# Kernel tuning notes

Measured on AMD Instinct MI355X. Metric: run time of the kernel, lower is better.

## Reference

```python
import jax, jax.numpy as jnp
import numpy as np

NUM_GROUPS = 512
GROUP_SIZE = 32
GROUP_RADIUS = 0.2
K_ORIGINAL = 5 * GROUP_SIZE  # ball_query oversampling factor from the source


def setup_inputs() -> dict:
    key = jax.random.key(0)
    k1, k2 = jax.random.split(key)
    B, N, C = 8, 16384, 4
    points = jax.random.normal(k1, (B, N, C), dtype=jnp.float32)
    # valid lengths in [N//2, N) so the lengths-masking path is exercised
    lengths = (N // 2 + jax.random.randint(k2, (B,), 0, N // 2)).astype(jnp.int32)
    return {"points": points, "lengths": lengths}


def _sample_farthest_points(xyz, lengths, K):
    # xyz: (B,N,3) float, lengths: (B,) int -> centers (B,K,3)
    B, N, _ = xyz.shape
    n_idx = jnp.arange(N)

    def per_batch(pts, length):
        valid = n_idx < length

        def step(carry, _):
            mindist, cur = carry
            d = jnp.sum((pts - pts[cur]) ** 2, axis=-1)  # (N,)
            mindist = jnp.where(valid, jnp.minimum(mindist, d), -jnp.inf)
            nxt = jnp.argmax(mindist).astype(jnp.int32)
            return (mindist, nxt), cur

        mindist0 = jnp.where(valid, jnp.inf, -jnp.inf)
        # deterministic start at index 0 (source uses random_start_point=True)
        (_, _), sel = jax.lax.scan(step, (mindist0, jnp.int32(0)), None, length=K)
        return pts[sel]

    return jax.vmap(per_batch)(xyz, lengths)


def _ball_query(centers, xyz, lengths, K, radius):
    # returns first-K (by point index, matching pytorch3d ball_query) indices
    # within radius; -1 padding. centers (B,G,3), xyz (B,N,3) -> idx (B,G,K)
    B, G, _ = centers.shape
    N = xyz.shape[1]
    d2 = jnp.sum((centers[:, :, None, :] - xyz[:, None, :, :]) ** 2, axis=-1)  # (B,G,N)
    valid = (jnp.arange(N) < lengths[:, None])[:, None, :]  # (B,1,N)
    mask = (d2 < radius * radius) & valid
    # score N-n > 0 iff in ball; top_k picks smallest indices first (in order)
    score = jnp.where(mask, N - jnp.arange(N, dtype=jnp.int32), jnp.int32(-1))
    vals, _ = jax.lax.top_k(score, K)
    return jnp.where(vals > 0, N - vals, -1)  # (B,G,K)


def _select_topk_by_energy(points, idx, K_new):
    # points (B,N,C), idx (B,G,K_orig) with -1 invalid -> (B,G,K_new)
    B, G, _ = idx.shape
    N = points.shape[1]
    invalid = idx == -1
    idxc = jnp.maximum(idx, 0)
    energies = jnp.broadcast_to(points[:, None, :, 3], (B, G, N))
    e = jnp.take_along_axis(energies, idxc, axis=2)  # (B,G,K_orig)
    e = jnp.where(invalid, -jnp.inf, e)
    top_e, top_i = jax.lax.top_k(e, K_new)
    topk_idx = jnp.take_along_axis(idx, top_i, axis=2)
    return jnp.where(top_e == -jnp.inf, -1, topk_idx)


def _masked_gather(points, idx):
    # points (B,N,C), idx (B,G,K); -1 -> gathered value 0.0 (pytorch3d semantics)
    B, G, K = idx.shape
    C = points.shape[-1]
    valid = idx >= 0
    flat = jnp.maximum(idx, 0).reshape(B, G * K)
    g = jnp.take_along_axis(points, flat[:, :, None], axis=1).reshape(B, G, K, C)
    return jnp.where(valid[..., None], g, 0.0)


def _forward(points, lengths):
    xyz = points[:, :, :3]
    centers = _sample_farthest_points(xyz, lengths, NUM_GROUPS)  # (B,G,3)
    idx = _ball_query(centers, xyz, lengths, K_ORIGINAL, GROUP_RADIUS)
    idx = _select_topk_by_energy(points, idx, GROUP_SIZE)  # (B,G,K)
    # fill_empty_indices: replace -1 with first index of the group
    first = idx[:, :, :1]
    idx = jnp.where(idx == -1, first, idx)
    groups = _masked_gather(points, idx)  # (B,G,K,C)
    groups = jnp.concatenate(
        [groups[..., :3] - centers[:, :, None, :], groups[..., 3:]], axis=-1
    )
    groups = groups / GROUP_RADIUS
    return groups, centers


def reference(points, lengths):
    return _forward(points, lengths)
```

## Files before the change

### kernel.cpp

```cpp
#include <hip/hip_runtime.h>

constexpr int B_ = 8;
constexpr int N_ = 16384;
constexpr int NG = 512;
constexpr int GS = 32;
constexpr int KORIG = 160;
constexpr int TPB = 1024;
constexpr int PPT = 16;
#define R2 0.04f
#define RADIUS 0.2f

typedef __attribute__((ext_vector_type(2))) float f32x2;
typedef __attribute__((ext_vector_type(4))) float f32x4;

__device__ __forceinline__ unsigned f32_ord(float f) {
  unsigned u = __float_as_uint(f);
  return (u & 0x80000000u) ? ~u : (u | 0x80000000u);
}

__device__ __forceinline__ f32x2 pk_add(f32x2 a, f32x2 b) {
  f32x2 d;
  asm("v_pk_add_f32 %0, %1, %2" : "=v"(d) : "v"(a), "v"(b));
  return d;
}
__device__ __forceinline__ f32x2 pk_mul(f32x2 a, f32x2 b) {
  f32x2 d;
  asm("v_pk_mul_f32 %0, %1, %2" : "=v"(d) : "v"(a), "v"(b));
  return d;
}

template <int CTRL>
__device__ __forceinline__ float dpp_fmax(float v) {
  int o = __builtin_amdgcn_update_dpp(0, __float_as_int(v), CTRL, 0xF, 0xF, true);
  return fmaxf(v, __int_as_float(o));
}
__device__ __forceinline__ float wave_fmax(float v) {
  v = dpp_fmax<0xB1>(v);
  v = dpp_fmax<0x4E>(v);
  v = dpp_fmax<0x141>(v);
  v = dpp_fmax<0x140>(v);
  v = fmaxf(v, __int_as_float(__builtin_amdgcn_ds_swizzle(__float_as_int(v), 0x401F)));
  v = fmaxf(v, __shfl_xor(v, 32, 64));
  return v;
}
__device__ __forceinline__ float group16_fmax(float v) {
  v = dpp_fmax<0xB1>(v);
  v = dpp_fmax<0x4E>(v);
  v = dpp_fmax<0x141>(v);
  v = dpp_fmax<0x140>(v);
  return v;
}

__global__ __launch_bounds__(1024, 4) void fps_kernel(const float4* __restrict__ p4,
                                                      const int* __restrict__ lengths,
                                                      float* __restrict__ centers) {
#pragma clang fp contract(off)
  const int b = blockIdx.x;
  const int t = threadIdx.x;
  const int lane = t & 63;
  const int wid = t >> 6;
  const int len = lengths[b];
  const float4* bp = p4 + (size_t)b * N_;
  const float INF = __builtin_inff();

  __shared__ f32x4 sxy4[16 * 8 * 64];
  __shared__ float pubf[2][16];
  __shared__ int pubi[2][16];

  const int base4 = wid * 512 + lane;

  f32x2 z2[8], m2[8];
#pragma unroll
  for (int p = 0; p < 8; ++p) {
    const int i0 = t * PPT + 2 * p;
    float4 a = bp[i0];
    float4 c = bp[i0 + 1];
    sxy4[base4 + p * 64] = (f32x4){a.x, c.x, a.y, c.y};
    z2[p] = (f32x2){a.z, c.z};
    m2[p].x = (i0 < len) ? INF : -INF;
    m2[p].y = (i0 + 1 < len) ? INF : -INF;
  }
  __syncthreads();

  float4 c0 = bp[0];
  float cx = c0.x, cy = c0.y, cz = c0.z;
  if (t == 0) {
    size_t o = (size_t)b * NG * 3;
    centers[o] = cx; centers[o + 1] = cy; centers[o + 2] = cz;
  }

  for (int k = 0; k < NG - 1; ++k) {
    const f32x2 mcx = {-cx, -cx};
    const f32x2 mcy = {-cy, -cy};
    const f32x2 mcz = {-cz, -cz};
#pragma unroll
    for (int p = 0; p < 8; ++p) {
      f32x4 q = sxy4[base4 + p * 64];
      f32x2 xx = pk_add(q.xy, mcx);
      f32x2 yy = pk_add(q.zw, mcy);
      f32x2 zz = pk_add(z2[p], mcz);
      f32x2 x2 = pk_mul(xx, xx);
      f32x2 y2 = pk_mul(yy, yy);
      f32x2 s1 = pk_add(x2, y2);
      f32x2 zq = pk_mul(zz, zz);
      f32x2 d2 = pk_add(s1, zq);
      m2[p].x = fminf(m2[p].x, d2.x);
      m2[p].y = fminf(m2[p].y, d2.y);
    }
    float p0 = fmaxf(m2[0].x, m2[0].y), p1 = fmaxf(m2[1].x, m2[1].y);
    float p2 = fmaxf(m2[2].x, m2[2].y), p3 = fmaxf(m2[3].x, m2[3].y);
    float p4_ = fmaxf(m2[4].x, m2[4].y), p5 = fmaxf(m2[5].x, m2[5].y);
    float p6 = fmaxf(m2[6].x, m2[6].y), p7 = fmaxf(m2[7].x, m2[7].y);
    float r0 = fmaxf(p0, p1), r1 = fmaxf(p2, p3);
    float r2 = fmaxf(p4_, p5), r3 = fmaxf(p6, p7);
    float s0 = fmaxf(r0, r1), s1 = fmaxf(r2, r3);
    const float sm = fmaxf(s0, s1);

    const bool bA = (s0 != sm);
    const float rA = bA ? r2 : r0;
    const bool bB = (rA != sm);
    const float qA = bA ? (bB ? p6 : p4_) : (bB ? p2 : p0);
    const bool bC = (qA != sm);
    const int jp = ((int)bA << 2) | ((int)bB << 1) | (int)bC;
    const float xlo = bA ? (bB ? (bC ? m2[7].x : m2[6].x) : (bC ? m2[5].x : m2[4].x))
                         : (bB ? (bC ? m2[3].x : m2[2].x) : (bC ? m2[1].x : m2[0].x));
    const bool blo = (xlo != sm);
    const int bj = (jp << 1) | (int)blo;

    const float wmax = wave_fmax(sm);
    const unsigned long long att = __ballot(sm == wmax);
    const int wl = __ffsll(att) - 1;
    if (lane == wl) {
      pubf[k & 1][wid] = wmax;
      pubi[k & 1][wid] = t * PPT + bj;
    }
    __syncthreads();

    const float pw = pubf[k & 1][lane & 15];
    const float kmax = group16_fmax(pw);
    const unsigned long long bal = __ballot(pw == kmax);
    const int grp = lane & 48;
    const int ww = __ffsll((bal >> grp) & 0xFFFFull) - 1;
    const int nxt = pubi[k & 1][ww];
    const int snxt = __builtin_amdgcn_readfirstlane(nxt);
    const float4 c = bp[snxt];
    cx = c.x; cy = c.y; cz = c.z;

    if (t == 0) {
      size_t o = ((size_t)b * NG + (k + 1)) * 3;
      centers[o] = cx; centers[o + 1] = cy; centers[o + 2] = cz;
    }
  }
}

__global__ __launch_bounds__(64) void group_kernel(const float4* __restrict__ p4,
                                                   const int* __restrict__ lengths,
                                                   const float* __restrict__ centers,
                                                   float4* __restrict__ outg) {
#pragma clang fp contract(off)
  const int gid = blockIdx.x;
  const int b = gid >> 9;
  const int lane = threadIdx.x;
  const int len = lengths[b];
  const float4* bp = p4 + (size_t)b * N_;
  const float cx = centers[(size_t)gid * 3 + 0];
  const float cy = centers[(size_t)gid * 3 + 1];
  const float cz = centers[(size_t)gid * 3 + 2];

  __shared__ int cand[KORIG];
  int M = 0;
  for (int cb = 0; cb < N_ && M < KORIG; cb += 256) {
#pragma unroll
    for (int q = 0; q < 4; ++q) {
      const int i = cb + q * 64 + lane;
      float4 p = bp[i];
      float dx = p.x - cx;
      float dy = p.y - cy;
      float dz = p.z - cz;
      float d2 = dx * dx + dy * dy + dz * dz;
      const bool pred = (i < len) && (d2 < R2);
      unsigned long long mb = __ballot(pred);
      if (pred) {
        int pos = M + (int)__popcll(mb & ((1ull << lane) - 1ull));
        if (pos < KORIG) cand[pos] = i;
      }
      M += (int)__popcll(mb);
    }
  }
  if (M > KORIG) M = KORIG;
  __syncthreads();

  const unsigned long long SENT = ~0ull;
  unsigned long long key0 = SENT, key1 = SENT, key2 = SENT;
  {
    int c0 = lane, c1 = lane + 64, c2 = lane + 128;
    if (c0 < M) { int i = cand[c0]; key0 = ((unsigned long long)(~f32_ord(bp[i].w)) << 32) | (unsigned)i; }
    if (c1 < M) { int i = cand[c1]; key1 = ((unsigned long long)(~f32_ord(bp[i].w)) << 32) | (unsigned)i; }
    if (c2 < M) { int i = cand[c2]; key2 = ((unsigned long long)(~f32_ord(bp[i].w)) << 32) | (unsigned)i; }
  }

  int mysel = -1;
  for (int j = 0; j < GS; ++j) {
    unsigned long long kmin = key0 < key1 ? key0 : key1;
    if (key2 < kmin) kmin = key2;
#pragma unroll
    for (int off = 32; off > 0; off >>= 1) {
      unsigned long long o = __shfl_xor(kmin, off, 64);
      if (o < kmin) kmin = o;
    }
    if (kmin == SENT) break;
    if (lane == j) mysel = (int)(unsigned)kmin;
    if (key0 == kmin) key0 = SENT;
    if (key1 == kmin) key1 = SENT;
    if (key2 == kmin) key2 = SENT;
  }

  const int first = __shfl(mysel, 0, 64);
  if (lane < GS) {
    int idx = (mysel < 0) ? first : mysel;
    float4 o;
    if (idx >= 0) {
      float4 p = bp[idx];
      o.x = (p.x - cx) / RADIUS;
      o.y = (p.y - cy) / RADIUS;
      o.z = (p.z - cz) / RADIUS;
      o.w = p.w / RADIUS;
    } else {
      o.x = (0.0f - cx) / RADIUS;
      o.y = (0.0f - cy) / RADIUS;
      o.z = (0.0f - cz) / RADIUS;
      o.w = 0.0f;
    }
    outg[(size_t)gid * GS + lane] = o;
  }
}

extern "C" void kernel_launch(void* const* d_in, const int* in_sizes, int n_in,
                              void* d_out, int out_size, void* d_ws, size_t ws_size,
                              hipStream_t stream) {
  const float4* pts = (const float4*)d_in[0];
  const int* lengths = (const int*)d_in[1];
  float* out = (float*)d_out;
  float* centers = out + (size_t)B_ * NG * GS * 4;
  float4* groups = (float4*)out;

  fps_kernel<<<B_, TPB, 0, stream>>>(pts, lengths, centers);
  group_kernel<<<B_ * NG, 64, 0, stream>>>(pts, lengths, centers, groups);
}
```

Baseline: 933.3 us.

## Publish winner coordinates through LDS instead of reloading the point from global memory

In the FPS loop, each wave's winning lane now writes its point's x, y, z coordinates (taken from registers and LDS) together with the max distance into a float4 in shared memory. The next center is then read with shuffles, so the dependent global load of bp[snxt] on the serial critical path of every iteration is gone. Center outputs are buffered in shared memory and written to global memory once after the loop, rather than by a single thread on every iteration. The cost is some extra per-iteration select logic and one more LDS read to fetch the winning coordinates.

```diff
diff --git a/kernel.cpp b/kernel.cpp
--- a/kernel.cpp
+++ b/kernel.cpp
@@ -64,8 +64,8 @@
   const float INF = __builtin_inff();
 
   __shared__ f32x4 sxy4[16 * 8 * 64];
-  __shared__ float pubf[2][16];
-  __shared__ int pubi[2][16];
+  __shared__ f32x4 pub4[2][16];
+  __shared__ float scen[NG * 3];
 
   const int base4 = wid * 512 + lane;
 
@@ -80,14 +80,13 @@
     m2[p].x = (i0 < len) ? INF : -INF;
     m2[p].y = (i0 + 1 < len) ? INF : -INF;
   }
-  __syncthreads();
 
   float4 c0 = bp[0];
   float cx = c0.x, cy = c0.y, cz = c0.z;
   if (t == 0) {
-    size_t o = (size_t)b * NG * 3;
-    centers[o] = cx; centers[o + 1] = cy; centers[o + 2] = cz;
-  }
+    scen[0] = cx; scen[1] = cy; scen[2] = cz;
+  }
+  __syncthreads();
 
   for (int k = 0; k < NG - 1; ++k) {
     const f32x2 mcx = {-cx, -cx};
@@ -125,32 +124,39 @@
     const float xlo = bA ? (bB ? (bC ? m2[7].x : m2[6].x) : (bC ? m2[5].x : m2[4].x))
                          : (bB ? (bC ? m2[3].x : m2[2].x) : (bC ? m2[1].x : m2[0].x));
     const bool blo = (xlo != sm);
-    const int bj = (jp << 1) | (int)blo;
+
+    f32x4 qq = sxy4[base4 + jp * 64];
+    const float gx = blo ? qq.y : qq.x;
+    const float gy = blo ? qq.w : qq.z;
+    const f32x2 zp = bA ? (bB ? (bC ? z2[7] : z2[6]) : (bC ? z2[5] : z2[4]))
+                        : (bB ? (bC ? z2[3] : z2[2]) : (bC ? z2[1] : z2[0]));
+    const float gz = blo ? zp.y : zp.x;
 
     const float wmax = wave_fmax(sm);
     const unsigned long long att = __ballot(sm == wmax);
     const int wl = __ffsll(att) - 1;
-    if (lane == wl) {
-      pubf[k & 1][wid] = wmax;
-      pubi[k & 1][wid] = t * PPT + bj;
-    }
+    if (lane == wl) pub4[k & 1][wid] = (f32x4){wmax, gx, gy, gz};
     __syncthreads();
 
-    const float pw = pubf[k & 1][lane & 15];
-    const float kmax = group16_fmax(pw);
-    const unsigned long long bal = __ballot(pw == kmax);
+    const f32x4 pv = pub4[k & 1][lane & 15];
+    const float kmax = group16_fmax(pv.x);
+    const unsigned long long bal = __ballot(pv.x == kmax);
     const int grp = lane & 48;
-    const int ww = __ffsll((bal >> grp) & 0xFFFFull) - 1;
-    const int nxt = pubi[k & 1][ww];
-    const int snxt = __builtin_amdgcn_readfirstlane(nxt);
-    const float4 c = bp[snxt];
-    cx = c.x; cy = c.y; cz = c.z;
+    const int src = grp + (__ffsll((bal >> grp) & 0xFFFFull) - 1);
+    cx = __shfl(pv.y, src, 64);
+    cy = __shfl(pv.z, src, 64);
+    cz = __shfl(pv.w, src, 64);
 
     if (t == 0) {
-      size_t o = ((size_t)b * NG + (k + 1)) * 3;
-      centers[o] = cx; centers[o + 1] = cy; centers[o + 2] = cz;
-    }
-  }
+      scen[(k + 1) * 3 + 0] = cx;
+      scen[(k + 1) * 3 + 1] = cy;
+      scen[(k + 1) * 3 + 2] = cz;
+    }
+  }
+  __syncthreads();
+
+  float* cb = centers + (size_t)b * NG * 3;
+  for (int i = t; i < NG * 3; i += TPB) cb[i] = scen[i];
 }
 
 __global__ __launch_bounds__(64) void group_kernel(const float4* __restrict__ p4,
```

Result: slower. 971.3 us (+4.1%).

## Shrink FPS block to four waves and replace barrier with tagged atomic publish

Applied to the files above, without the earlier changes.

The farthest-point-sampling kernel now runs 256 threads, each holding 64 points in registers instead of 16, which widens the per-thread reduction tree to 32 pairs. The per-iteration __syncthreads and 16-wave second-stage reduction are replaced by each wave atomically publishing a packed (ordered max, iteration tag, index) word. Waves spin until all four slots carry the current iteration tag. This aims to cut barrier and cross-wave reduction latency in the serial 511-step loop. In exchange there is less latency hiding per SIMD, much higher register pressure, and reliance on spin-wait memory ordering.

```diff
diff --git a/kernel.cpp b/kernel.cpp
--- a/kernel.cpp
+++ b/kernel.cpp
@@ -5,8 +5,8 @@
 constexpr int NG = 512;
 constexpr int GS = 32;
 constexpr int KORIG = 160;
-constexpr int TPB = 1024;
-constexpr int PPT = 16;
+constexpr int TPB = 256;
+constexpr int PPT = 64;
 #define R2 0.04f
 #define RADIUS 0.2f
 
@@ -33,6 +33,11 @@
 __device__ __forceinline__ float dpp_fmax(float v) {
   int o = __builtin_amdgcn_update_dpp(0, __float_as_int(v), CTRL, 0xF, 0xF, true);
   return fmaxf(v, __int_as_float(o));
+}
+template <int CTRL>
+__device__ __forceinline__ unsigned dpp_umax(unsigned v) {
+  int o = __builtin_amdgcn_update_dpp(0, (int)v, CTRL, 0xF, 0xF, true);
+  return v > (unsigned)o ? v : (unsigned)o;
 }
 __device__ __forceinline__ float wave_fmax(float v) {
   v = dpp_fmax<0xB1>(v);
@@ -43,17 +48,12 @@
   v = fmaxf(v, __shfl_xor(v, 32, 64));
   return v;
 }
-__device__ __forceinline__ float group16_fmax(float v) {
-  v = dpp_fmax<0xB1>(v);
-  v = dpp_fmax<0x4E>(v);
-  v = dpp_fmax<0x141>(v);
-  v = dpp_fmax<0x140>(v);
-  return v;
-}
-
-__global__ __launch_bounds__(1024, 4) void fps_kernel(const float4* __restrict__ p4,
-                                                      const int* __restrict__ lengths,
-                                                      float* __restrict__ centers) {
+
+__global__ __attribute__((amdgpu_flat_work_group_size(256, 256),
+                          amdgpu_waves_per_eu(1, 1)))
+void fps_kernel(const float4* __restrict__ p4,
+                const int* __restrict__ lengths,
+                float* __restrict__ centers) {
 #pragma clang fp contract(off)
   const int b = blockIdx.x;
   const int t = threadIdx.x;
@@ -63,15 +63,14 @@
   const float4* bp = p4 + (size_t)b * N_;
   const float INF = __builtin_inff();
 
-  __shared__ f32x4 sxy4[16 * 8 * 64];
-  __shared__ float pubf[2][16];
-  __shared__ int pubi[2][16];
-
-  const int base4 = wid * 512 + lane;
-
-  f32x2 z2[8], m2[8];
-#pragma unroll
-  for (int p = 0; p < 8; ++p) {
+  __shared__ f32x4 sxy4[32 * 4 * 64];
+  __shared__ unsigned long long pub[2][4];
+
+  const int base4 = wid * 2048 + lane;
+
+  f32x2 z2[32], m2[32];
+#pragma unroll
+  for (int p = 0; p < 32; ++p) {
     const int i0 = t * PPT + 2 * p;
     float4 a = bp[i0];
     float4 c = bp[i0 + 1];
@@ -80,6 +79,7 @@
     m2[p].x = (i0 < len) ? INF : -INF;
     m2[p].y = (i0 + 1 < len) ? INF : -INF;
   }
+  if (t < 8) ((unsigned long long*)pub)[t] = ~0ull;
   __syncthreads();
 
   float4 c0 = bp[0];
@@ -94,7 +94,7 @@
     const f32x2 mcy = {-cy, -cy};
     const f32x2 mcz = {-cz, -cz};
 #pragma unroll
-    for (int p = 0; p < 8; ++p) {
+    for (int p = 0; p < 32; ++p) {
       f32x4 q = sxy4[base4 + p * 64];
       f32x2 xx = pk_add(q.xy, mcx);
       f32x2 yy = pk_add(q.zw, mcy);
@@ -107,42 +107,74 @@
       m2[p].x = fminf(m2[p].x, d2.x);
       m2[p].y = fminf(m2[p].y, d2.y);
     }
-    float p0 = fmaxf(m2[0].x, m2[0].y), p1 = fmaxf(m2[1].x, m2[1].y);
-    float p2 = fmaxf(m2[2].x, m2[2].y), p3 = fmaxf(m2[3].x, m2[3].y);
-    float p4_ = fmaxf(m2[4].x, m2[4].y), p5 = fmaxf(m2[5].x, m2[5].y);
-    float p6 = fmaxf(m2[6].x, m2[6].y), p7 = fmaxf(m2[7].x, m2[7].y);
-    float r0 = fmaxf(p0, p1), r1 = fmaxf(p2, p3);
-    float r2 = fmaxf(p4_, p5), r3 = fmaxf(p6, p7);
-    float s0 = fmaxf(r0, r1), s1 = fmaxf(r2, r3);
-    const float sm = fmaxf(s0, s1);
-
-    const bool bA = (s0 != sm);
-    const float rA = bA ? r2 : r0;
-    const bool bB = (rA != sm);
-    const float qA = bA ? (bB ? p6 : p4_) : (bB ? p2 : p0);
-    const bool bC = (qA != sm);
-    const int jp = ((int)bA << 2) | ((int)bB << 1) | (int)bC;
-    const float xlo = bA ? (bB ? (bC ? m2[7].x : m2[6].x) : (bC ? m2[5].x : m2[4].x))
-                         : (bB ? (bC ? m2[3].x : m2[2].x) : (bC ? m2[1].x : m2[0].x));
-    const bool blo = (xlo != sm);
-    const int bj = (jp << 1) | (int)blo;
+    float a32[32];
+#pragma unroll
+    for (int i = 0; i < 32; ++i) a32[i] = fmaxf(m2[i].x, m2[i].y);
+    float a16[16];
+#pragma unroll
+    for (int i = 0; i < 16; ++i) a16[i] = fmaxf(a32[2 * i], a32[2 * i + 1]);
+    float a8[8];
+#pragma unroll
+    for (int i = 0; i < 8; ++i) a8[i] = fmaxf(a16[2 * i], a16[2 * i + 1]);
+    float a4[4];
+#pragma unroll
+    for (int i = 0; i < 4; ++i) a4[i] = fmaxf(a8[2 * i], a8[2 * i + 1]);
+    float a2[2] = {fmaxf(a4[0], a4[1]), fmaxf(a4[2], a4[3])};
+    const float sm = fmaxf(a2[0], a2[1]);
+
+    const bool i1 = (a2[0] != sm);
+    const float aL4 = i1 ? a4[2] : a4[0];
+    const bool i2 = (aL4 != sm);
+    const float aL8 = i1 ? (i2 ? a8[6] : a8[4]) : (i2 ? a8[2] : a8[0]);
+    const bool i3 = (aL8 != sm);
+    const float aL16 = i1 ? (i2 ? (i3 ? a16[14] : a16[12]) : (i3 ? a16[10] : a16[8]))
+                          : (i2 ? (i3 ? a16[6] : a16[4]) : (i3 ? a16[2] : a16[0]));
+    const bool i4 = (aL16 != sm);
+    const float aL32 =
+        i1 ? (i2 ? (i3 ? (i4 ? a32[30] : a32[28]) : (i4 ? a32[26] : a32[24]))
+                 : (i3 ? (i4 ? a32[22] : a32[20]) : (i4 ? a32[18] : a32[16])))
+           : (i2 ? (i3 ? (i4 ? a32[14] : a32[12]) : (i4 ? a32[10] : a32[8]))
+                 : (i3 ? (i4 ? a32[6] : a32[4]) : (i4 ? a32[2] : a32[0])));
+    const bool i5 = (aL32 != sm);
+    const int jp = ((int)i1 << 4) | ((int)i2 << 3) | ((int)i3 << 2) |
+                   ((int)i4 << 1) | (int)i5;
+    const float mlo =
+        i1 ? (i2 ? (i3 ? (i4 ? (i5 ? m2[31].x : m2[30].x) : (i5 ? m2[29].x : m2[28].x))
+                       : (i4 ? (i5 ? m2[27].x : m2[26].x) : (i5 ? m2[25].x : m2[24].x)))
+                 : (i3 ? (i4 ? (i5 ? m2[23].x : m2[22].x) : (i5 ? m2[21].x : m2[20].x))
+                       : (i4 ? (i5 ? m2[19].x : m2[18].x) : (i5 ? m2[17].x : m2[16].x))))
+           : (i2 ? (i3 ? (i4 ? (i5 ? m2[15].x : m2[14].x) : (i5 ? m2[13].x : m2[12].x))
+                       : (i4 ? (i5 ? m2[11].x : m2[10].x) : (i5 ? m2[9].x : m2[8].x)))
+                 : (i3 ? (i4 ? (i5 ? m2[7].x : m2[6].x) : (i5 ? m2[5].x : m2[4].x))
+                       : (i4 ? (i5 ? m2[3].x : m2[2].x) : (i5 ? m2[1].x : m2[0].x))));
+    const bool blo = (mlo != sm);
+    const int gidx = t * PPT + jp * 2 + (int)blo;
 
     const float wmax = wave_fmax(sm);
     const unsigned long long att = __ballot(sm == wmax);
     const int wl = __ffsll(att) - 1;
+
     if (lane == wl) {
-      pubf[k & 1][wid] = wmax;
-      pubi[k & 1][wid] = t * PPT + bj;
-    }
-    __syncthreads();
-
-    const float pw = pubf[k & 1][lane & 15];
-    const float kmax = group16_fmax(pw);
-    const unsigned long long bal = __ballot(pw == kmax);
-    const int grp = lane & 48;
-    const int ww = __ffsll((bal >> grp) & 0xFFFFull) - 1;
-    const int nxt = pubi[k & 1][ww];
-    const int snxt = __builtin_amdgcn_readfirstlane(nxt);
+      unsigned long long val = ((unsigned long long)f32_ord(wmax) << 32) |
+                               (unsigned)((k << 14) | gidx);
+      __hip_atomic_store(&pub[k & 1][wid], val, __ATOMIC_RELEASE,
+                         __HIP_MEMORY_SCOPE_WORKGROUP);
+    }
+    unsigned long long pv = 0;
+    const bool po = lane < 4;
+    for (;;) {
+      if (po) pv = __hip_atomic_load(&pub[k & 1][lane], __ATOMIC_ACQUIRE,
+                                     __HIP_MEMORY_SCOPE_WORKGROUP);
+      const bool ok = !po || (((unsigned)pv >> 14) == (unsigned)k);
+      if (__all(ok)) break;
+    }
+    const unsigned o0 = po ? (unsigned)(pv >> 32) : 0u;
+    unsigned km = dpp_umax<0xB1>(o0);
+    km = dpp_umax<0x4E>(km);
+    const unsigned long long bal = __ballot(po && (o0 == km)) & 0xFull;
+    const int src = __ffsll(bal) - 1;
+    const int gsel = __shfl((int)((unsigned)pv & 0x3FFFu), src, 64);
+    const int snxt = __builtin_amdgcn_readfirstlane(gsel);
     const float4 c = bp[snxt];
     cx = c.x; cy = c.y; cz = c.z;
 
```

New measurement: 1.163 ms. 1.25x slower.

## Halve FPS block size and keep all point coordinates in registers

Applied to the files above, without the earlier changes.

The farthest-point-sampling kernel now runs 512 threads per block with 32 points per thread. All x/y/z coordinates live in registers instead of being re-read from LDS on every iteration. The cross-wave reduction shrinks to 8 waves and uses a shuffle to fetch the winning index instead of an LDS read. This removes per-iteration LDS traffic in the serial 511-step loop and shortens the reduction, in exchange for more registers per thread, half as many threads, and a longer per-thread argmax selection tree.

```diff
diff --git a/kernel.cpp b/kernel.cpp
--- a/kernel.cpp
+++ b/kernel.cpp
@@ -5,13 +5,12 @@
 constexpr int NG = 512;
 constexpr int GS = 32;
 constexpr int KORIG = 160;
-constexpr int TPB = 1024;
-constexpr int PPT = 16;
+constexpr int TPB = 512;
+constexpr int PPT = 32;
 #define R2 0.04f
 #define RADIUS 0.2f
 
 typedef __attribute__((ext_vector_type(2))) float f32x2;
-typedef __attribute__((ext_vector_type(4))) float f32x4;
 
 __device__ __forceinline__ unsigned f32_ord(float f) {
   unsigned u = __float_as_uint(f);
@@ -43,17 +42,18 @@
   v = fmaxf(v, __shfl_xor(v, 32, 64));
   return v;
 }
-__device__ __forceinline__ float group16_fmax(float v) {
+__device__ __forceinline__ float group8_fmax(float v) {
   v = dpp_fmax<0xB1>(v);
   v = dpp_fmax<0x4E>(v);
   v = dpp_fmax<0x141>(v);
-  v = dpp_fmax<0x140>(v);
   return v;
 }
 
-__global__ __launch_bounds__(1024, 4) void fps_kernel(const float4* __restrict__ p4,
-                                                      const int* __restrict__ lengths,
-                                                      float* __restrict__ centers) {
+__global__ __attribute__((amdgpu_flat_work_group_size(512, 512),
+                          amdgpu_waves_per_eu(2, 2)))
+void fps_kernel(const float4* __restrict__ p4,
+                const int* __restrict__ lengths,
+                float* __restrict__ centers) {
 #pragma clang fp contract(off)
   const int b = blockIdx.x;
   const int t = threadIdx.x;
@@ -63,24 +63,21 @@
   const float4* bp = p4 + (size_t)b * N_;
   const float INF = __builtin_inff();
 
-  __shared__ f32x4 sxy4[16 * 8 * 64];
-  __shared__ float pubf[2][16];
-  __shared__ int pubi[2][16];
-
-  const int base4 = wid * 512 + lane;
-
-  f32x2 z2[8], m2[8];
-#pragma unroll
-  for (int p = 0; p < 8; ++p) {
+  __shared__ float pubf[2][8];
+  __shared__ int pubi[2][8];
+
+  f32x2 x2[16], y2[16], z2[16], m2[16];
+#pragma unroll
+  for (int p = 0; p < 16; ++p) {
     const int i0 = t * PPT + 2 * p;
     float4 a = bp[i0];
     float4 c = bp[i0 + 1];
-    sxy4[base4 + p * 64] = (f32x4){a.x, c.x, a.y, c.y};
+    x2[p] = (f32x2){a.x, c.x};
+    y2[p] = (f32x2){a.y, c.y};
     z2[p] = (f32x2){a.z, c.z};
     m2[p].x = (i0 < len) ? INF : -INF;
     m2[p].y = (i0 + 1 < len) ? INF : -INF;
   }
-  __syncthreads();
 
   float4 c0 = bp[0];
   float cx = c0.x, cy = c0.y, cz = c0.z;
@@ -94,55 +91,64 @@
     const f32x2 mcy = {-cy, -cy};
     const f32x2 mcz = {-cz, -cz};
 #pragma unroll
-    for (int p = 0; p < 8; ++p) {
-      f32x4 q = sxy4[base4 + p * 64];
-      f32x2 xx = pk_add(q.xy, mcx);
-      f32x2 yy = pk_add(q.zw, mcy);
+    for (int p = 0; p < 16; ++p) {
+      f32x2 xx = pk_add(x2[p], mcx);
+      f32x2 yy = pk_add(y2[p], mcy);
       f32x2 zz = pk_add(z2[p], mcz);
-      f32x2 x2 = pk_mul(xx, xx);
-      f32x2 y2 = pk_mul(yy, yy);
-      f32x2 s1 = pk_add(x2, y2);
-      f32x2 zq = pk_mul(zz, zz);
-      f32x2 d2 = pk_add(s1, zq);
+      f32x2 xs = pk_mul(xx, xx);
+      f32x2 ys = pk_mul(yy, yy);
+      f32x2 s1 = pk_add(xs, ys);
+      f32x2 zs = pk_mul(zz, zz);
+      f32x2 d2 = pk_add(s1, zs);
       m2[p].x = fminf(m2[p].x, d2.x);
       m2[p].y = fminf(m2[p].y, d2.y);
     }
-    float p0 = fmaxf(m2[0].x, m2[0].y), p1 = fmaxf(m2[1].x, m2[1].y);
-    float p2 = fmaxf(m2[2].x, m2[2].y), p3 = fmaxf(m2[3].x, m2[3].y);
-    float p4_ = fmaxf(m2[4].x, m2[4].y), p5 = fmaxf(m2[5].x, m2[5].y);
-    float p6 = fmaxf(m2[6].x, m2[6].y), p7 = fmaxf(m2[7].x, m2[7].y);
-    float r0 = fmaxf(p0, p1), r1 = fmaxf(p2, p3);
-    float r2 = fmaxf(p4_, p5), r3 = fmaxf(p6, p7);
-    float s0 = fmaxf(r0, r1), s1 = fmaxf(r2, r3);
-    const float sm = fmaxf(s0, s1);
-
-    const bool bA = (s0 != sm);
-    const float rA = bA ? r2 : r0;
-    const bool bB = (rA != sm);
-    const float qA = bA ? (bB ? p6 : p4_) : (bB ? p2 : p0);
-    const bool bC = (qA != sm);
-    const int jp = ((int)bA << 2) | ((int)bB << 1) | (int)bC;
-    const float xlo = bA ? (bB ? (bC ? m2[7].x : m2[6].x) : (bC ? m2[5].x : m2[4].x))
-                         : (bB ? (bC ? m2[3].x : m2[2].x) : (bC ? m2[1].x : m2[0].x));
-    const bool blo = (xlo != sm);
-    const int bj = (jp << 1) | (int)blo;
+    float pm[16];
+#pragma unroll
+    for (int i = 0; i < 16; ++i) pm[i] = fmaxf(m2[i].x, m2[i].y);
+    float b8[8];
+#pragma unroll
+    for (int i = 0; i < 8; ++i) b8[i] = fmaxf(pm[2 * i], pm[2 * i + 1]);
+    float b4[4];
+#pragma unroll
+    for (int i = 0; i < 4; ++i) b4[i] = fmaxf(b8[2 * i], b8[2 * i + 1]);
+    float b2[2] = {fmaxf(b4[0], b4[1]), fmaxf(b4[2], b4[3])};
+    const float sm = fmaxf(b2[0], b2[1]);
+
+    const bool i1 = (b2[0] != sm);
+    const float aL4 = i1 ? b4[2] : b4[0];
+    const bool i2 = (aL4 != sm);
+    const float aL8 = i1 ? (i2 ? b8[6] : b8[4]) : (i2 ? b8[2] : b8[0]);
+    const bool i3 = (aL8 != sm);
+    const float pmL = i1 ? (i2 ? (i3 ? pm[14] : pm[12]) : (i3 ? pm[10] : pm[8]))
+                         : (i2 ? (i3 ? pm[6] : pm[4]) : (i3 ? pm[2] : pm[0]));
+    const bool i4 = (pmL != sm);
+    const int jp = ((int)i1 << 3) | ((int)i2 << 2) | ((int)i3 << 1) | (int)i4;
+    const float mlo =
+        i1 ? (i2 ? (i3 ? (i4 ? m2[15].x : m2[14].x) : (i4 ? m2[13].x : m2[12].x))
+                 : (i3 ? (i4 ? m2[11].x : m2[10].x) : (i4 ? m2[9].x : m2[8].x)))
+           : (i2 ? (i3 ? (i4 ? m2[7].x : m2[6].x) : (i4 ? m2[5].x : m2[4].x))
+                 : (i3 ? (i4 ? m2[3].x : m2[2].x) : (i4 ? m2[1].x : m2[0].x)));
+    const bool blo = (mlo != sm);
+    const int gidx = t * PPT + jp * 2 + (int)blo;
 
     const float wmax = wave_fmax(sm);
     const unsigned long long att = __ballot(sm == wmax);
     const int wl = __ffsll(att) - 1;
     if (lane == wl) {
       pubf[k & 1][wid] = wmax;
-      pubi[k & 1][wid] = t * PPT + bj;
+      pubi[k & 1][wid] = gidx;
     }
     __syncthreads();
 
-    const float pw = pubf[k & 1][lane & 15];
-    const float kmax = group16_fmax(pw);
+    const float pw = pubf[k & 1][lane & 7];
+    const int pi = pubi[k & 1][lane & 7];
+    const float kmax = group8_fmax(pw);
     const unsigned long long bal = __ballot(pw == kmax);
-    const int grp = lane & 48;
-    const int ww = __ffsll((bal >> grp) & 0xFFFFull) - 1;
-    const int nxt = pubi[k & 1][ww];
-    const int snxt = __builtin_amdgcn_readfirstlane(nxt);
+    const int grp = lane & 56;
+    const int src = grp + (__ffsll((bal >> grp) & 0xFFull) - 1);
+    const int gsel = __shfl(pi, src, 64);
+    const int snxt = __builtin_amdgcn_readfirstlane(gsel);
     const float4 c = bp[snxt];
     cx = c.x; cy = c.y; cz = c.z;
 
```

After: 891.5 us, median of 2. 4.5% less time.
